# Optimization experiments

Measured on AMD Instinct MI355X. Metric: run time of the kernel, lower is better.

Reference implementation:

```python
import jax, jax.numpy as jnp
import numpy as np

EPS = 1e-5
HEADS = 8
SR = 4


def bn(x, gamma, beta, mean, var):
    # BatchNorm in inference form; channel axis = 1
    shape = (1, -1) + (1,) * (x.ndim - 2)
    inv = gamma.reshape(shape) / jnp.sqrt(var.reshape(shape) + EPS)
    return (x - mean.reshape(shape)) * inv + beta.reshape(shape)


def setup_inputs() -> dict:
    key = jax.random.key(0)
    ks = jax.random.split(key, 8)
    B, C, H, W = 2, 256, 128, 128
    N = H * W
    conv1d_std = np.sqrt(2.0 / C)            # fan_out = 1*C
    conv2d_std = np.sqrt(2.0 / (SR * SR * C))  # fan_out = sr*sr*C
    return {
        "x": jax.random.normal(ks[0], (B, C, N), dtype=jnp.float32),
        "w_q": jax.random.normal(ks[1], (C, C), dtype=jnp.float32) * conv1d_std,
        "w_k": jax.random.normal(ks[2], (C, C), dtype=jnp.float32) * conv1d_std,
        "w_sr": jax.random.normal(ks[3], (C, C, SR, SR), dtype=jnp.float32) * conv2d_std,
        "sr_gamma": jnp.ones((C,), jnp.float32),
        "sr_beta": jnp.zeros((C,), jnp.float32),
        "sr_mean": jnp.zeros((C,), jnp.float32),
        "sr_var": jnp.ones((C,), jnp.float32),
        "w_proj": jax.random.normal(ks[4], (C, C), dtype=jnp.float32) * conv1d_std,
        "proj_gamma": jnp.ones((C,), jnp.float32),
        "proj_beta": jnp.zeros((C,), jnp.float32),
        "proj_mean": jnp.zeros((C,), jnp.float32),
        "proj_var": jnp.ones((C,), jnp.float32),
        "H": 128,
        "W": 128,
    }


def reference(x, w_q, w_k, w_sr, sr_gamma, sr_beta, sr_mean, sr_var,
              w_proj, proj_gamma, proj_beta, proj_mean, proj_var, H, W):
    B, C, N = x.shape
    hd = C // HEADS
    scale = hd ** -0.5
    # q: Conv1d(k=1) == channel matmul -> (B, heads, N, hd)
    q = jnp.einsum('oc,bcn->bon', w_q, x).reshape(B, HEADS, hd, N).transpose(0, 1, 3, 2)
    # spatial reduction: Conv2d(k=SR, s=SR) as patch-reshape + einsum, then BN
    xp = x.reshape(B, C, H // SR, SR, W // SR, SR)
    xr = jnp.einsum('bchpwq,ocpq->bohw', xp, w_sr).reshape(B, C, (H // SR) * (W // SR))
    xr = bn(xr, sr_gamma, sr_beta, sr_mean, sr_var)
    # k: (B, heads, hd, N_kv)
    k = jnp.einsum('oc,bcm->bom', w_k, xr).reshape(B, HEADS, hd, -1)
    # scores (B, heads, N, N_kv) -> max over kv
    scores = jnp.einsum('bhnd,bhdm->bhnm', q, k) * scale
    attn = scores.max(axis=-1)                # (B, heads, N)
    # v = mean-pooled x, identical per head -> matmul collapses to sum over heads
    v = x.mean(axis=-1)                       # (B, C)
    out = jnp.einsum('bhn,bc->bcn', attn, v)  # (B, C, N)
    out = jnp.einsum('oc,bcn->bon', w_proj, out)
    return bn(out, proj_gamma, proj_beta, proj_mean, proj_var)
```

## Files before the change

### kernel.cpp

```cpp
#include <hip/hip_runtime.h>
#include <hip/hip_bf16.h>
#include <math.h>

#define EPSF 1e-5f
#define SCALE 0.17677669529663687f

typedef __bf16 bf16x8 __attribute__((ext_vector_type(8)));
typedef __bf16 bf16x4 __attribute__((ext_vector_type(4)));
typedef float f32x4 __attribute__((ext_vector_type(4)));


__global__ __launch_bounds__(256) void k_ab(const float* __restrict__ v,
                                            const float* __restrict__ wproj,
                                            const float* __restrict__ pg,
                                            const float* __restrict__ pb,
                                            const float* __restrict__ pm,
                                            const float* __restrict__ pvar,
                                            float* __restrict__ A,
                                            float* __restrict__ B0) {
    __shared__ float vl[256];
    int t = threadIdx.x, b = blockIdx.x;
    vl[t] = v[b * 256 + t] * (1.0f / 16384.0f);
    __syncthreads();
    const float* wr = wproj + t * 256;
    float s = 0.f;
#pragma unroll 8
    for (int c = 0; c < 256; c += 4) {
        float4 w = *(const float4*)&wr[c];
        s += w.x * vl[c] + w.y * vl[c + 1] + w.z * vl[c + 2] + w.w * vl[c + 3];
    }
    float inv = pg[t] / sqrtf(pvar[t] + EPSF);
    A[b * 256 + t] = s * inv;
    if (b == 0) B0[t] = pb[t] - pm[t] * inv;
}

__global__ __launch_bounds__(256) void k_wprep(const float* __restrict__ wq,
                                               const float* __restrict__ wk,
                                               const float* __restrict__ wsr,
                                               __bf16* __restrict__ wqf,
                                               __bf16* __restrict__ wkb,
                                               __bf16* __restrict__ wsrf,
                                               float* __restrict__ v) {
    int bi = blockIdx.x, t = threadIdx.x;
    if (bi < 32) {
        if (bi == 0) { v[t] = 0.f; v[256 + t] = 0.f; }
        int tt = bi * 256 + t;
        int o = tt >> 5, chunk = tt & 31;
        float4 v0 = *(const float4*)&wq[o * 256 + (chunk << 3)];
        float4 v1 = *(const float4*)&wq[o * 256 + (chunk << 3) + 4];
        bf16x8 p;
        p[0] = (__bf16)v0.x; p[1] = (__bf16)v0.y; p[2] = (__bf16)v0.z; p[3] = (__bf16)v0.w;
        p[4] = (__bf16)v1.x; p[5] = (__bf16)v1.y; p[6] = (__bf16)v1.z; p[7] = (__bf16)v1.w;
        int cc = chunk >> 2, quad = chunk & 3;
        *(bf16x8*)&wqf[(((((o >> 4) << 3) + cc) << 6) + (quad << 4) + (o & 15)) << 3] = p;
    } else if (bi < 64) {
        int e = (bi - 32) * 256 + t;
        float4 v0 = *(const float4*)&wk[e << 3];
        float4 v1 = *(const float4*)&wk[(e << 3) + 4];
        bf16x8 p;
        p[0] = (__bf16)(v0.x * SCALE); p[1] = (__bf16)(v0.y * SCALE);
        p[2] = (__bf16)(v0.z * SCALE); p[3] = (__bf16)(v0.w * SCALE);
        p[4] = (__bf16)(v1.x * SCALE); p[5] = (__bf16)(v1.y * SCALE);
        p[6] = (__bf16)(v1.z * SCALE); p[7] = (__bf16)(v1.w * SCALE);
        *(bf16x8*)&wkb[e << 3] = p;
    } else {
        int tt = (bi - 64) * 256 + t;
        int o = tt >> 9, chunk = tt & 511;
        float4 v0 = *(const float4*)&wsr[o * 4096 + (chunk << 3)];
        float4 v1 = *(const float4*)&wsr[o * 4096 + (chunk << 3) + 4];
        bf16x8 p;
        p[0] = (__bf16)v0.x; p[1] = (__bf16)v0.y; p[2] = (__bf16)v0.z; p[3] = (__bf16)v0.w;
        p[4] = (__bf16)v1.x; p[5] = (__bf16)v1.y; p[6] = (__bf16)v1.z; p[7] = (__bf16)v1.w;
        int cc = chunk >> 2, quad = chunk & 3;
        *(bf16x8*)&wsrf[(((((o >> 4) << 7) + cc) << 6) + (quad << 4) + (o & 15)) << 3] = p;
    }
}

__global__ __launch_bounds__(256) void k_im2col(const float* __restrict__ x,
                                                __bf16* __restrict__ Pbf,
                                                float* __restrict__ v) {
    __shared__ float csum[32];
    int t = threadIdx.x, bid = blockIdx.x;
    int b = bid >> 8, hm = (bid >> 3) & 31, ccg = bid & 7;
    int wm = t >> 3, c8 = t & 7;
    if (t < 32) csum[t] = 0.f;
    __syncthreads();
    const int mtile = (hm << 1) + (wm >> 4);
    const int ln = wm & 15;
#pragma unroll
    for (int cci = 0; cci < 4; ++cci) {
        int c = (ccg << 5) + (cci << 3) + c8;
        const float* src = x + ((size_t)(b * 256 + c) << 14) + (hm << 9) + (wm << 2);
        bf16x8 o0, o1;
        float s = 0.f;
#pragma unroll
        for (int p = 0; p < 2; ++p) {
            float4 vv = *(const float4*)&src[p << 7];
            s += vv.x + vv.y + vv.z + vv.w;
            o0[p * 4 + 0] = (__bf16)vv.x; o0[p * 4 + 1] = (__bf16)vv.y;
            o0[p * 4 + 2] = (__bf16)vv.z; o0[p * 4 + 3] = (__bf16)vv.w;
        }
#pragma unroll
        for (int p = 0; p < 2; ++p) {
            float4 vv = *(const float4*)&src[(p + 2) << 7];
            s += vv.x + vv.y + vv.z + vv.w;
            o1[p * 4 + 0] = (__bf16)vv.x; o1[p * 4 + 1] = (__bf16)vv.y;
            o1[p * 4 + 2] = (__bf16)vv.z; o1[p * 4 + 3] = (__bf16)vv.w;
        }
        size_t d0 = (((((size_t)(b * 64 + mtile) << 7) + (c >> 1)) << 6) +
                     (((c & 1) << 1) << 4) + ln) << 3;
        *(bf16x8*)&Pbf[d0] = o0;
        *(bf16x8*)&Pbf[d0 + 128] = o1;
        atomicAdd(&csum[(cci << 3) + c8], s);
    }
    __syncthreads();
    if (t < 32) atomicAdd(&v[b * 256 + (ccg << 5) + t], csum[t]);
}

__global__ __launch_bounds__(256) void k_conv1(const __bf16* __restrict__ Pbf,
                                               const __bf16* __restrict__ wsrf,
                                               float* __restrict__ xrp) {
    const int t = threadIdx.x, bid = blockIdx.x;
    const int b = bid & 1, mt = (bid >> 1) & 63, ks = bid >> 7;
    const int w = t >> 6, lane = t & 63, ln = lane & 15, quad = lane >> 4;
    f32x4 acc[4];
#pragma unroll
    for (int ot = 0; ot < 4; ++ot) acc[ot] = (f32x4){0.f, 0.f, 0.f, 0.f};
    const __bf16* pa = Pbf + ((((size_t)(b * 64 + mt) << 7) + (ks << 5)) << 9) + (lane << 3);
    const __bf16* pbm = wsrf + ((((size_t)(w << 2) << 7) + (ks << 5)) << 9) + (lane << 3);
#pragma unroll 4
    for (int cci = 0; cci < 32; ++cci) {
        const int cb = cci << 9;
        bf16x8 af = *(const bf16x8*)&pa[cb];
        bf16x8 bfr[4];
#pragma unroll
        for (int ot = 0; ot < 4; ++ot) bfr[ot] = *(const bf16x8*)&pbm[(ot << 16) + cb];
#pragma unroll
        for (int ot = 0; ot < 4; ++ot)
            acc[ot] = __builtin_amdgcn_mfma_f32_16x16x32_bf16(af, bfr[ot], acc[ot], 0, 0, 0);
    }
    float* dst = xrp + ((size_t)((ks << 1) + b) << 18);
#pragma unroll
    for (int ot = 0; ot < 4; ++ot)
#pragma unroll
        for (int r = 0; r < 4; ++r) {
            int m = (mt << 4) + (quad << 2) + r;
            int o = (w << 6) + (ot << 4) + ln;
            dst[m * 256 + o] = acc[ot][r];
        }
}

__global__ __launch_bounds__(256) void k_comb2(const float* __restrict__ xrp,
                                               const float* __restrict__ sg,
                                               const float* __restrict__ sb,
                                               const float* __restrict__ smn,
                                               const float* __restrict__ svar,
                                               __bf16* __restrict__ xrb) {
    int t = threadIdx.x, bid = blockIdx.x;
    int b = bid >> 8, m = ((bid & 255) << 2) + (t >> 6);
    int o4 = (t & 63) << 2;
    size_t base = (((size_t)b << 10) + m) << 8;
    float4 s0 = *(const float4*)&xrp[base + o4];
    float4 s1 = *(const float4*)&xrp[524288 + base + o4];
    float4 s2 = *(const float4*)&xrp[1048576 + base + o4];
    float4 s3 = *(const float4*)&xrp[1572864 + base + o4];
    float4 g = *(const float4*)&sg[o4];
    float4 vr = *(const float4*)&svar[o4];
    float4 mn = *(const float4*)&smn[o4];
    float4 bt = *(const float4*)&sb[o4];
    bf16x4 r;
    r[0] = (__bf16)((s0.x + s1.x + s2.x + s3.x - mn.x) * (g.x / sqrtf(vr.x + EPSF)) + bt.x);
    r[1] = (__bf16)((s0.y + s1.y + s2.y + s3.y - mn.y) * (g.y / sqrtf(vr.y + EPSF)) + bt.y);
    r[2] = (__bf16)((s0.z + s1.z + s2.z + s3.z - mn.z) * (g.z / sqrtf(vr.z + EPSF)) + bt.z);
    r[3] = (__bf16)((s0.w + s1.w + s2.w + s3.w - mn.w) * (g.w / sqrtf(vr.w + EPSF)) + bt.w);
    *(bf16x4*)&xrb[base + o4] = r;
}

__global__ __launch_bounds__(256) void k_kmat2(const __bf16* __restrict__ xrb,
                                               const __bf16* __restrict__ wkb,
                                               __bf16* __restrict__ kkbh) {
    const int t = threadIdx.x, bid = blockIdx.x;
    const int b = bid >> 6, mt = bid & 63;
    const int w = t >> 6, lane = t & 63, ln = lane & 15, quad = lane >> 4;
    f32x4 acc[4];
#pragma unroll
    for (int ot = 0; ot < 4; ++ot) acc[ot] = (f32x4){0.f, 0.f, 0.f, 0.f};
    const __bf16* pa = xrb + ((((size_t)b << 10) + (mt << 4) + ln) << 8) + (quad << 3);
    const __bf16* pbm = wkb + (((w << 6) + ln) << 8) + (quad << 3);
#pragma unroll
    for (int cc = 0; cc < 8; ++cc) {
        const int cb = cc << 5;
        bf16x8 af = *(const bf16x8*)&pa[cb];
        bf16x8 bfr[4];
#pragma unroll
        for (int ot = 0; ot < 4; ++ot) bfr[ot] = *(const bf16x8*)&pbm[(ot << 12) + cb];
#pragma unroll
        for (int ot = 0; ot < 4; ++ot)
            acc[ot] = __builtin_amdgcn_mfma_f32_16x16x32_bf16(af, bfr[ot], acc[ot], 0, 0, 0);
    }
#pragma unroll
    for (int ot = 0; ot < 4; ++ot)
#pragma unroll
        for (int r = 0; r < 4; ++r) {
            int m = (mt << 4) + (quad << 2) + r;
            int h = (w << 1) + (ot >> 1);
            int d = ((ot & 1) << 4) + ln;
            kkbh[(((size_t)(b * 8 + h)) << 15) + (m << 5) + d] = (__bf16)acc[ot][r];
        }
}

__global__ __launch_bounds__(256) void k_xt(const float* __restrict__ x,
                                            __bf16* __restrict__ xTf) {
    __shared__ float ts[32 * 68];
    int t = threadIdx.x, bid = blockIdx.x;
    int b = bid >> 8, n0 = (bid & 255) << 6;
    const int nl = t >> 2;
    const int ch = (t & 3) << 3;
    const int n = n0 + nl;
    const int ntile = n >> 4, ln = n & 15, quad = ch >> 3;
    const int cl = t >> 3;
    const int n8 = (t & 7) << 3;
    for (int s8 = 0; s8 < 8; ++s8) {
        int c0 = s8 << 5;
        __syncthreads();
        {
            const float* src = &x[((size_t)(b * 256 + c0 + cl) << 14) + n0 + n8];
            *(float4*)&ts[cl * 68 + n8] = *(const float4*)&src[0];
            *(float4*)&ts[cl * 68 + n8 + 4] = *(const float4*)&src[4];
        }
        __syncthreads();
        bf16x8 p;
#pragma unroll
        for (int j = 0; j < 8; ++j) p[j] = (__bf16)ts[(ch + j) * 68 + nl];
        *(bf16x8*)&xTf[(((((size_t)(b * 1024 + ntile) << 3) + s8) << 6) +
                        (quad << 4) + ln) << 3] = p;
    }
}

__global__ __launch_bounds__(256) void k_scores2(const __bf16* __restrict__ xTf,
                                                 const __bf16* __restrict__ wqf,
                                                 const __bf16* __restrict__ kkbh,
                                                 const float* __restrict__ A,
                                                 const float* __restrict__ B0,
                                                 float* __restrict__ out) {
    __shared__ __align__(16) __bf16 qs[64 * 264];
    __shared__ float smax[2048];
    __shared__ float ss[64];
    __shared__ float sA[256], sB[256];
    const int t = threadIdx.x;
    const int w = t >> 6;
    const int lane = t & 63;
    const int ln = lane & 15;
    const int quad = lane >> 4;
    const int b = blockIdx.x >> 8;
    const int n0 = (blockIdx.x & 255) << 6;

    f32x4 acc[4][4];
#pragma unroll
    for (int nt = 0; nt < 4; ++nt)
#pragma unroll
        for (int ot = 0; ot < 4; ++ot) acc[nt][ot] = (f32x4){0.f, 0.f, 0.f, 0.f};
    const __bf16* pa = xTf + (((size_t)(b * 1024 + (n0 >> 4))) << 12) + (lane << 3);
    const __bf16* pbm = wqf + ((size_t)w << 14) + (lane << 3);
#pragma unroll 2
    for (int cc = 0; cc < 8; ++cc) {
        const int cb = cc << 9;
        bf16x8 af[4], bfr[4];
#pragma unroll
        for (int nt = 0; nt < 4; ++nt) af[nt] = *(const bf16x8*)&pa[(nt << 12) + cb];
#pragma unroll
        for (int ot = 0; ot < 4; ++ot) bfr[ot] = *(const bf16x8*)&pbm[(ot << 12) + cb];
#pragma unroll
        for (int nt = 0; nt < 4; ++nt)
#pragma unroll
            for (int ot = 0; ot < 4; ++ot)
                acc[nt][ot] = __builtin_amdgcn_mfma_f32_16x16x32_bf16(af[nt], bfr[ot],
                                                                      acc[nt][ot], 0, 0, 0);
    }
#pragma unroll
    for (int nt = 0; nt < 4; ++nt)
#pragma unroll
        for (int ot = 0; ot < 4; ++ot)
#pragma unroll
            for (int r = 0; r < 4; ++r)
                qs[((nt << 4) + (quad << 2) + r) * 264 + (w << 6) + (ot << 4) + ln] =
                    (__bf16)acc[nt][ot][r];
    __syncthreads();

    const f32x4 zf = {0.f, 0.f, 0.f, 0.f};
    for (int h = 0; h < 8; ++h) {
        bf16x8 qb[4];
#pragma unroll
        for (int nt = 0; nt < 4; ++nt)
            qb[nt] = *(const bf16x8*)&qs[((nt << 4) + ln) * 264 + (h << 5) + (quad << 3)];
        const __bf16* kb_base = kkbh + ((size_t)(b * 8 + h) << 15) + (ln << 5) + (quad << 3);
        bf16x8 kb[16];
#pragma unroll
        for (int i = 0; i < 16; ++i)
            kb[i] = *(const bf16x8*)&kb_base[((w << 8) + (i << 4)) << 5];
        float rmx[4] = {-INFINITY, -INFINITY, -INFINITY, -INFINITY};
#pragma unroll
        for (int i = 0; i < 16; ++i)
#pragma unroll
            for (int nt = 0; nt < 4; ++nt) {
                f32x4 d = __builtin_amdgcn_mfma_f32_16x16x32_bf16(kb[i], qb[nt], zf, 0, 0, 0);
                rmx[nt] = fmaxf(rmx[nt], fmaxf(fmaxf(d[0], d[1]), fmaxf(d[2], d[3])));
            }
#pragma unroll
        for (int nt = 0; nt < 4; ++nt) {
            rmx[nt] = fmaxf(rmx[nt], __shfl_xor(rmx[nt], 16, 64));
            rmx[nt] = fmaxf(rmx[nt], __shfl_xor(rmx[nt], 32, 64));
        }
        if (lane < 16) {
#pragma unroll
            for (int nt = 0; nt < 4; ++nt)
                smax[(w << 9) + (h << 6) + (nt << 4) + lane] = rmx[nt];
        }
    }
    __syncthreads();
    if (t < 64) {
        float ssum = 0.f;
#pragma unroll
        for (int h = 0; h < 8; ++h) {
            float vv = fmaxf(fmaxf(smax[(h << 6) + t], smax[512 + (h << 6) + t]),
                             fmaxf(smax[1024 + (h << 6) + t], smax[1536 + (h << 6) + t]));
            ssum += vv;
        }
        ss[t] = ssum;
    }
    sA[t] = A[b * 256 + t];
    sB[t] = B0[t];
    __syncthreads();

#pragma unroll
    for (int i = 0; i < 16; ++i) {
        int e = t + (i << 8);
        int c = e >> 4, n4 = (e & 15) << 2;
        float4 s4 = *(const float4*)&ss[n4];
        float a = sA[c], bb = sB[c];
        float4 o4 = make_float4(fmaf(a, s4.x, bb), fmaf(a, s4.y, bb),
                                fmaf(a, s4.z, bb), fmaf(a, s4.w, bb));
        *(float4*)&out[((size_t)(b * 256 + c) << 14) + n0 + n4] = o4;
    }
}

extern "C" void kernel_launch(void* const* d_in, const int* in_sizes, int n_in,
                              void* d_out, int out_size, void* d_ws, size_t ws_size,
                              hipStream_t stream) {
    const float* x    = (const float*)d_in[0];
    const float* wq   = (const float*)d_in[1];
    const float* wk   = (const float*)d_in[2];
    const float* wsr  = (const float*)d_in[3];
    const float* sg   = (const float*)d_in[4];
    const float* sb   = (const float*)d_in[5];
    const float* smn  = (const float*)d_in[6];
    const float* svr  = (const float*)d_in[7];
    const float* wproj= (const float*)d_in[8];
    const float* pg   = (const float*)d_in[9];
    const float* pb   = (const float*)d_in[10];
    const float* pm   = (const float*)d_in[11];
    const float* pvr  = (const float*)d_in[12];
    float* out = (float*)d_out;

    char* W = (char*)d_ws;
    float*  w_v   = (float*) (W + 0);
    float*  w_A   = (float*) (W + 4096);
    float*  w_B0  = (float*) (W + 8192);
    __bf16* w_wqf = (__bf16*)(W + 16384);
    __bf16* w_wkb = (__bf16*)(W + 147456);
    __bf16* w_wsrf= (__bf16*)(W + 278528);
    __bf16* w_xrb = (__bf16*)(W + 2375680);
    __bf16* w_kkbh= (__bf16*)(W + 2899968);
    float*  w_xrp = (float*) (W + 3948544);
    __bf16* w_Pbf = (__bf16*)(W + 12337152);
    __bf16* w_xTf = (__bf16*)(W + 12337152);

    k_wprep<<<576, 256, 0, stream>>>(wq, wk, wsr, w_wqf, w_wkb, w_wsrf, w_v);
    k_im2col<<<512, 256, 0, stream>>>(x, w_Pbf, w_v);
    k_ab<<<2, 256, 0, stream>>>(w_v, wproj, pg, pb, pm, pvr, w_A, w_B0);
    k_conv1<<<512, 256, 0, stream>>>(w_Pbf, w_wsrf, w_xrp);
    k_comb2<<<512, 256, 0, stream>>>(w_xrp, sg, sb, smn, svr, w_xrb);
    k_kmat2<<<128, 256, 0, stream>>>(w_xrb, w_wkb, w_kkbh);
    k_xt<<<512, 256, 0, stream>>>(x, w_xTf);
    k_scores2<<<512, 256, 0, stream>>>(w_xTf, w_wqf, w_kkbh, w_A, w_B0, out);
}
```

Before: 194.8 us.

## Merge staging kernels, fuse conv BN, split scores by head pairs

Merges im2col and the x transpose into one launch, and folds the projection-vector kernel into the k-matrix kernel. The conv now runs its full K reduction per block with BN applied in the epilogue, which removes the fp32 partial buffer and the combine kernel. Scores are split four ways across head pairs to raise block count, with per-head maxima summed through global atomics into a zeroed buffer. A separate epilogue kernel then writes the output. The cost is that each head-pair block recomputes the q projection for its slice, and atomics plus an extra launch are added.

```diff
diff --git a/kernel.cpp b/kernel.cpp
--- a/kernel.cpp
+++ b/kernel.cpp
@@ -9,30 +9,6 @@
 typedef __bf16 bf16x4 __attribute__((ext_vector_type(4)));
 typedef float f32x4 __attribute__((ext_vector_type(4)));
 
-
-__global__ __launch_bounds__(256) void k_ab(const float* __restrict__ v,
-                                            const float* __restrict__ wproj,
-                                            const float* __restrict__ pg,
-                                            const float* __restrict__ pb,
-                                            const float* __restrict__ pm,
-                                            const float* __restrict__ pvar,
-                                            float* __restrict__ A,
-                                            float* __restrict__ B0) {
-    __shared__ float vl[256];
-    int t = threadIdx.x, b = blockIdx.x;
-    vl[t] = v[b * 256 + t] * (1.0f / 16384.0f);
-    __syncthreads();
-    const float* wr = wproj + t * 256;
-    float s = 0.f;
-#pragma unroll 8
-    for (int c = 0; c < 256; c += 4) {
-        float4 w = *(const float4*)&wr[c];
-        s += w.x * vl[c] + w.y * vl[c + 1] + w.z * vl[c + 2] + w.w * vl[c + 3];
-    }
-    float inv = pg[t] / sqrtf(pvar[t] + EPSF);
-    A[b * 256 + t] = s * inv;
-    if (b == 0) B0[t] = pb[t] - pm[t] * inv;
-}
 
 __global__ __launch_bounds__(256) void k_wprep(const float* __restrict__ wq,
                                                const float* __restrict__ wk,
@@ -40,8 +16,14 @@
                                                __bf16* __restrict__ wqf,
                                                __bf16* __restrict__ wkb,
                                                __bf16* __restrict__ wsrf,
-                                               float* __restrict__ v) {
+                                               float* __restrict__ v,
+                                               float* __restrict__ ssg) {
     int bi = blockIdx.x, t = threadIdx.x;
+    if (bi >= 576) {
+        int e = (bi - 576) * 256 + t;
+        *(float4*)&ssg[e << 2] = make_float4(0.f, 0.f, 0.f, 0.f);
+        return;
+    }
     if (bi < 32) {
         if (bi == 0) { v[t] = 0.f; v[256 + t] = 0.f; }
         int tt = bi * 256 + t;
@@ -76,110 +58,134 @@
     }
 }
 
-__global__ __launch_bounds__(256) void k_im2col(const float* __restrict__ x,
-                                                __bf16* __restrict__ Pbf,
-                                                float* __restrict__ v) {
-    __shared__ float csum[32];
-    int t = threadIdx.x, bid = blockIdx.x;
-    int b = bid >> 8, hm = (bid >> 3) & 31, ccg = bid & 7;
-    int wm = t >> 3, c8 = t & 7;
-    if (t < 32) csum[t] = 0.f;
-    __syncthreads();
-    const int mtile = (hm << 1) + (wm >> 4);
-    const int ln = wm & 15;
-#pragma unroll
-    for (int cci = 0; cci < 4; ++cci) {
-        int c = (ccg << 5) + (cci << 3) + c8;
-        const float* src = x + ((size_t)(b * 256 + c) << 14) + (hm << 9) + (wm << 2);
-        bf16x8 o0, o1;
-        float s = 0.f;
-#pragma unroll
-        for (int p = 0; p < 2; ++p) {
-            float4 vv = *(const float4*)&src[p << 7];
-            s += vv.x + vv.y + vv.z + vv.w;
-            o0[p * 4 + 0] = (__bf16)vv.x; o0[p * 4 + 1] = (__bf16)vv.y;
-            o0[p * 4 + 2] = (__bf16)vv.z; o0[p * 4 + 3] = (__bf16)vv.w;
-        }
-#pragma unroll
-        for (int p = 0; p < 2; ++p) {
-            float4 vv = *(const float4*)&src[(p + 2) << 7];
-            s += vv.x + vv.y + vv.z + vv.w;
-            o1[p * 4 + 0] = (__bf16)vv.x; o1[p * 4 + 1] = (__bf16)vv.y;
-            o1[p * 4 + 2] = (__bf16)vv.z; o1[p * 4 + 3] = (__bf16)vv.w;
-        }
-        size_t d0 = (((((size_t)(b * 64 + mtile) << 7) + (c >> 1)) << 6) +
-                     (((c & 1) << 1) << 4) + ln) << 3;
-        *(bf16x8*)&Pbf[d0] = o0;
-        *(bf16x8*)&Pbf[d0 + 128] = o1;
-        atomicAdd(&csum[(cci << 3) + c8], s);
-    }
-    __syncthreads();
-    if (t < 32) atomicAdd(&v[b * 256 + (ccg << 5) + t], csum[t]);
-}
-
-__global__ __launch_bounds__(256) void k_conv1(const __bf16* __restrict__ Pbf,
-                                               const __bf16* __restrict__ wsrf,
-                                               float* __restrict__ xrp) {
+__global__ __launch_bounds__(256) void k_stage(const float* __restrict__ x,
+                                               __bf16* __restrict__ Pbf,
+                                               __bf16* __restrict__ xTf,
+                                               float* __restrict__ v) {
+    int t = threadIdx.x, bid0 = blockIdx.x;
+    if (bid0 < 512) {
+        __shared__ float csum[32];
+        int bid = bid0;
+        int b = bid >> 8, hm = (bid >> 3) & 31, ccg = bid & 7;
+        int wm = t >> 3, c8 = t & 7;
+        if (t < 32) csum[t] = 0.f;
+        __syncthreads();
+        const int mtile = (hm << 1) + (wm >> 4);
+        const int ln = wm & 15;
+#pragma unroll
+        for (int cci = 0; cci < 4; ++cci) {
+            int c = (ccg << 5) + (cci << 3) + c8;
+            const float* src = x + ((size_t)(b * 256 + c) << 14) + (hm << 9) + (wm << 2);
+            bf16x8 o0, o1;
+            float s = 0.f;
+#pragma unroll
+            for (int p = 0; p < 2; ++p) {
+                float4 vv = *(const float4*)&src[p << 7];
+                s += vv.x + vv.y + vv.z + vv.w;
+                o0[p * 4 + 0] = (__bf16)vv.x; o0[p * 4 + 1] = (__bf16)vv.y;
+                o0[p * 4 + 2] = (__bf16)vv.z; o0[p * 4 + 3] = (__bf16)vv.w;
+            }
+#pragma unroll
+            for (int p = 0; p < 2; ++p) {
+                float4 vv = *(const float4*)&src[(p + 2) << 7];
+                s += vv.x + vv.y + vv.z + vv.w;
+                o1[p * 4 + 0] = (__bf16)vv.x; o1[p * 4 + 1] = (__bf16)vv.y;
+                o1[p * 4 + 2] = (__bf16)vv.z; o1[p * 4 + 3] = (__bf16)vv.w;
+            }
+            size_t d0 = (((((size_t)(b * 64 + mtile) << 7) + (c >> 1)) << 6) +
+                         (((c & 1) << 1) << 4) + ln) << 3;
+            *(bf16x8*)&Pbf[d0] = o0;
+            *(bf16x8*)&Pbf[d0 + 128] = o1;
+            atomicAdd(&csum[(cci << 3) + c8], s);
+        }
+        __syncthreads();
+        if (t < 32) atomicAdd(&v[b * 256 + (ccg << 5) + t], csum[t]);
+    } else {
+        __shared__ float ts[32 * 68];
+        int bid = bid0 - 512;
+        int b = bid >> 8, n0 = (bid & 255) << 6;
+        const int nl = t >> 2;
+        const int ch = (t & 3) << 3;
+        const int n = n0 + nl;
+        const int ntile = n >> 4, ln = n & 15, quad = ch >> 3;
+        const int cl = t >> 3;
+        const int n8 = (t & 7) << 3;
+        for (int s8 = 0; s8 < 8; ++s8) {
+            int c0 = s8 << 5;
+            __syncthreads();
+            {
+                const float* src = &x[((size_t)(b * 256 + c0 + cl) << 14) + n0 + n8];
+                *(float4*)&ts[cl * 68 + n8] = *(const float4*)&src[0];
+                *(float4*)&ts[cl * 68 + n8 + 4] = *(const float4*)&src[4];
+            }
+            __syncthreads();
+            bf16x8 p;
+#pragma unroll
+            for (int j = 0; j < 8; ++j) p[j] = (__bf16)ts[(ch + j) * 68 + nl];
+            *(bf16x8*)&xTf[(((((size_t)(b * 1024 + ntile) << 3) + s8) << 6) +
+                            (quad << 4) + ln) << 3] = p;
+        }
+    }
+}
+
+__global__ __launch_bounds__(256) void k_conv1f(const __bf16* __restrict__ Pbf,
+                                                const __bf16* __restrict__ wsrf,
+                                                const float* __restrict__ sg,
+                                                const float* __restrict__ sb,
+                                                const float* __restrict__ smn,
+                                                const float* __restrict__ svar,
+                                                __bf16* __restrict__ xrb) {
     const int t = threadIdx.x, bid = blockIdx.x;
-    const int b = bid & 1, mt = (bid >> 1) & 63, ks = bid >> 7;
+    const int b = bid & 1, mt = (bid >> 1) & 63, og = bid >> 7;
     const int w = t >> 6, lane = t & 63, ln = lane & 15, quad = lane >> 4;
-    f32x4 acc[4];
-#pragma unroll
-    for (int ot = 0; ot < 4; ++ot) acc[ot] = (f32x4){0.f, 0.f, 0.f, 0.f};
-    const __bf16* pa = Pbf + ((((size_t)(b * 64 + mt) << 7) + (ks << 5)) << 9) + (lane << 3);
-    const __bf16* pbm = wsrf + ((((size_t)(w << 2) << 7) + (ks << 5)) << 9) + (lane << 3);
-#pragma unroll 4
-    for (int cci = 0; cci < 32; ++cci) {
-        const int cb = cci << 9;
-        bf16x8 af = *(const bf16x8*)&pa[cb];
-        bf16x8 bfr[4];
-#pragma unroll
-        for (int ot = 0; ot < 4; ++ot) bfr[ot] = *(const bf16x8*)&pbm[(ot << 16) + cb];
-#pragma unroll
-        for (int ot = 0; ot < 4; ++ot)
-            acc[ot] = __builtin_amdgcn_mfma_f32_16x16x32_bf16(af, bfr[ot], acc[ot], 0, 0, 0);
-    }
-    float* dst = xrp + ((size_t)((ks << 1) + b) << 18);
-#pragma unroll
-    for (int ot = 0; ot < 4; ++ot)
-#pragma unroll
-        for (int r = 0; r < 4; ++r) {
-            int m = (mt << 4) + (quad << 2) + r;
-            int o = (w << 6) + (ot << 4) + ln;
-            dst[m * 256 + o] = acc[ot][r];
-        }
-}
-
-__global__ __launch_bounds__(256) void k_comb2(const float* __restrict__ xrp,
-                                               const float* __restrict__ sg,
-                                               const float* __restrict__ sb,
-                                               const float* __restrict__ smn,
-                                               const float* __restrict__ svar,
-                                               __bf16* __restrict__ xrb) {
-    int t = threadIdx.x, bid = blockIdx.x;
-    int b = bid >> 8, m = ((bid & 255) << 2) + (t >> 6);
-    int o4 = (t & 63) << 2;
-    size_t base = (((size_t)b << 10) + m) << 8;
-    float4 s0 = *(const float4*)&xrp[base + o4];
-    float4 s1 = *(const float4*)&xrp[524288 + base + o4];
-    float4 s2 = *(const float4*)&xrp[1048576 + base + o4];
-    float4 s3 = *(const float4*)&xrp[1572864 + base + o4];
-    float4 g = *(const float4*)&sg[o4];
-    float4 vr = *(const float4*)&svar[o4];
-    float4 mn = *(const float4*)&smn[o4];
-    float4 bt = *(const float4*)&sb[o4];
-    bf16x4 r;
-    r[0] = (__bf16)((s0.x + s1.x + s2.x + s3.x - mn.x) * (g.x / sqrtf(vr.x + EPSF)) + bt.x);
-    r[1] = (__bf16)((s0.y + s1.y + s2.y + s3.y - mn.y) * (g.y / sqrtf(vr.y + EPSF)) + bt.y);
-    r[2] = (__bf16)((s0.z + s1.z + s2.z + s3.z - mn.z) * (g.z / sqrtf(vr.z + EPSF)) + bt.z);
-    r[3] = (__bf16)((s0.w + s1.w + s2.w + s3.w - mn.w) * (g.w / sqrtf(vr.w + EPSF)) + bt.w);
-    *(bf16x4*)&xrb[base + o4] = r;
+    f32x4 acc = (f32x4){0.f, 0.f, 0.f, 0.f};
+    const __bf16* pa = Pbf + ((size_t)(b * 64 + mt) << 16) + (lane << 3);
+    const __bf16* pbm = wsrf + ((size_t)(og * 4 + w) << 16) + (lane << 3);
+#pragma unroll 8
+    for (int cc = 0; cc < 128; ++cc) {
+        bf16x8 af = *(const bf16x8*)&pa[cc << 9];
+        bf16x8 bf = *(const bf16x8*)&pbm[cc << 9];
+        acc = __builtin_amdgcn_mfma_f32_16x16x32_bf16(af, bf, acc, 0, 0, 0);
+    }
+    const int o = (og << 6) + (w << 4) + ln;
+    float inv = sg[o] / sqrtf(svar[o] + EPSF);
+    float mn = smn[o], bt = sb[o];
+#pragma unroll
+    for (int r = 0; r < 4; ++r) {
+        int m = (mt << 4) + (quad << 2) + r;
+        xrb[(((size_t)b << 10) + m) * 256 + o] = (__bf16)((acc[r] - mn) * inv + bt);
+    }
 }
 
 __global__ __launch_bounds__(256) void k_kmat2(const __bf16* __restrict__ xrb,
                                                const __bf16* __restrict__ wkb,
-                                               __bf16* __restrict__ kkbh) {
+                                               __bf16* __restrict__ kkbh,
+                                               const float* __restrict__ v,
+                                               const float* __restrict__ wproj,
+                                               const float* __restrict__ pg,
+                                               const float* __restrict__ pb,
+                                               const float* __restrict__ pm,
+                                               const float* __restrict__ pvar,
+                                               float* __restrict__ A,
+                                               float* __restrict__ B0) {
     const int t = threadIdx.x, bid = blockIdx.x;
+    if (bid >= 128) {
+        __shared__ float vl[256];
+        int b = bid - 128;
+        vl[t] = v[b * 256 + t] * (1.0f / 16384.0f);
+        __syncthreads();
+        const float* wr = wproj + t * 256;
+        float s = 0.f;
+#pragma unroll 8
+        for (int c = 0; c < 256; c += 4) {
+            float4 w4 = *(const float4*)&wr[c];
+            s += w4.x * vl[c] + w4.y * vl[c + 1] + w4.z * vl[c + 2] + w4.w * vl[c + 3];
+        }
+        float inv = pg[t] / sqrtf(pvar[t] + EPSF);
+        A[b * 256 + t] = s * inv;
+        if (b == 0) B0[t] = pb[t] - pm[t] * inv;
+        return;
+    }
     const int b = bid >> 6, mt = bid & 63;
     const int w = t >> 6, lane = t & 63, ln = lane & 15, quad = lane >> 4;
     f32x4 acc[4];
@@ -209,90 +215,53 @@
         }
 }
 
-__global__ __launch_bounds__(256) void k_xt(const float* __restrict__ x,
-                                            __bf16* __restrict__ xTf) {
-    __shared__ float ts[32 * 68];
-    int t = threadIdx.x, bid = blockIdx.x;
-    int b = bid >> 8, n0 = (bid & 255) << 6;
-    const int nl = t >> 2;
-    const int ch = (t & 3) << 3;
-    const int n = n0 + nl;
-    const int ntile = n >> 4, ln = n & 15, quad = ch >> 3;
-    const int cl = t >> 3;
-    const int n8 = (t & 7) << 3;
-    for (int s8 = 0; s8 < 8; ++s8) {
-        int c0 = s8 << 5;
-        __syncthreads();
-        {
-            const float* src = &x[((size_t)(b * 256 + c0 + cl) << 14) + n0 + n8];
-            *(float4*)&ts[cl * 68 + n8] = *(const float4*)&src[0];
-            *(float4*)&ts[cl * 68 + n8 + 4] = *(const float4*)&src[4];
-        }
-        __syncthreads();
-        bf16x8 p;
-#pragma unroll
-        for (int j = 0; j < 8; ++j) p[j] = (__bf16)ts[(ch + j) * 68 + nl];
-        *(bf16x8*)&xTf[(((((size_t)(b * 1024 + ntile) << 3) + s8) << 6) +
-                        (quad << 4) + ln) << 3] = p;
-    }
-}
-
 __global__ __launch_bounds__(256) void k_scores2(const __bf16* __restrict__ xTf,
                                                  const __bf16* __restrict__ wqf,
                                                  const __bf16* __restrict__ kkbh,
-                                                 const float* __restrict__ A,
-                                                 const float* __restrict__ B0,
-                                                 float* __restrict__ out) {
-    __shared__ __align__(16) __bf16 qs[64 * 264];
-    __shared__ float smax[2048];
-    __shared__ float ss[64];
-    __shared__ float sA[256], sB[256];
+                                                 float* __restrict__ ssg) {
+    __shared__ __align__(16) __bf16 qs[64 * 72];
+    __shared__ float smax[512];
     const int t = threadIdx.x;
     const int w = t >> 6;
     const int lane = t & 63;
     const int ln = lane & 15;
     const int quad = lane >> 4;
-    const int b = blockIdx.x >> 8;
-    const int n0 = (blockIdx.x & 255) << 6;
-
-    f32x4 acc[4][4];
-#pragma unroll
-    for (int nt = 0; nt < 4; ++nt)
-#pragma unroll
-        for (int ot = 0; ot < 4; ++ot) acc[nt][ot] = (f32x4){0.f, 0.f, 0.f, 0.f};
-    const __bf16* pa = xTf + (((size_t)(b * 1024 + (n0 >> 4))) << 12) + (lane << 3);
-    const __bf16* pbm = wqf + ((size_t)w << 14) + (lane << 3);
+    const int bx = blockIdx.x;
+    const int hp = bx & 3;
+    const int n0 = ((bx >> 2) & 255) << 6;
+    const int b = bx >> 10;
+
+    f32x4 acc[4];
+#pragma unroll
+    for (int ot = 0; ot < 4; ++ot) acc[ot] = (f32x4){0.f, 0.f, 0.f, 0.f};
+    const __bf16* pa = xTf + ((size_t)(b * 1024 + (n0 >> 4) + w) << 12) + (lane << 3);
+    const __bf16* pbm = wqf + ((size_t)(hp << 2) << 12) + (lane << 3);
 #pragma unroll 2
     for (int cc = 0; cc < 8; ++cc) {
         const int cb = cc << 9;
-        bf16x8 af[4], bfr[4];
-#pragma unroll
-        for (int nt = 0; nt < 4; ++nt) af[nt] = *(const bf16x8*)&pa[(nt << 12) + cb];
+        bf16x8 af = *(const bf16x8*)&pa[cb];
+        bf16x8 bfr[4];
 #pragma unroll
         for (int ot = 0; ot < 4; ++ot) bfr[ot] = *(const bf16x8*)&pbm[(ot << 12) + cb];
 #pragma unroll
+        for (int ot = 0; ot < 4; ++ot)
+            acc[ot] = __builtin_amdgcn_mfma_f32_16x16x32_bf16(af, bfr[ot], acc[ot], 0, 0, 0);
+    }
+#pragma unroll
+    for (int ot = 0; ot < 4; ++ot)
+#pragma unroll
+        for (int r = 0; r < 4; ++r)
+            qs[((w << 4) + (quad << 2) + r) * 72 + (ot << 4) + ln] = (__bf16)acc[ot][r];
+    __syncthreads();
+
+    const f32x4 zf = {0.f, 0.f, 0.f, 0.f};
+#pragma unroll
+    for (int hl = 0; hl < 2; ++hl) {
+        const int h = (hp << 1) + hl;
+        bf16x8 qb[4];
+#pragma unroll
         for (int nt = 0; nt < 4; ++nt)
-#pragma unroll
-            for (int ot = 0; ot < 4; ++ot)
-                acc[nt][ot] = __builtin_amdgcn_mfma_f32_16x16x32_bf16(af[nt], bfr[ot],
-                                                                      acc[nt][ot], 0, 0, 0);
-    }
-#pragma unroll
-    for (int nt = 0; nt < 4; ++nt)
-#pragma unroll
-        for (int ot = 0; ot < 4; ++ot)
-#pragma unroll
-            for (int r = 0; r < 4; ++r)
-                qs[((nt << 4) + (quad << 2) + r) * 264 + (w << 6) + (ot << 4) + ln] =
-                    (__bf16)acc[nt][ot][r];
-    __syncthreads();
-
-    const f32x4 zf = {0.f, 0.f, 0.f, 0.f};
-    for (int h = 0; h < 8; ++h) {
-        bf16x8 qb[4];
-#pragma unroll
-        for (int nt = 0; nt < 4; ++nt)
-            qb[nt] = *(const bf16x8*)&qs[((nt << 4) + ln) * 264 + (h << 5) + (quad << 3)];
+            qb[nt] = *(const bf16x8*)&qs[((nt << 4) + ln) * 72 + (hl << 5) + (quad << 3)];
         const __bf16* kb_base = kkbh + ((size_t)(b * 8 + h) << 15) + (ln << 5) + (quad << 3);
         bf16x8 kb[16];
 #pragma unroll
@@ -304,7 +273,8 @@
 #pragma unroll
             for (int nt = 0; nt < 4; ++nt) {
                 f32x4 d = __builtin_amdgcn_mfma_f32_16x16x32_bf16(kb[i], qb[nt], zf, 0, 0, 0);
-                rmx[nt] = fmaxf(rmx[nt], fmaxf(fmaxf(d[0], d[1]), fmaxf(d[2], d[3])));
+                float t1 = fmaxf(fmaxf(d[0], d[1]), d[2]);
+                rmx[nt] = fmaxf(fmaxf(t1, d[3]), rmx[nt]);
             }
 #pragma unroll
         for (int nt = 0; nt < 4; ++nt) {
@@ -314,24 +284,29 @@
         if (lane < 16) {
 #pragma unroll
             for (int nt = 0; nt < 4; ++nt)
-                smax[(w << 9) + (h << 6) + (nt << 4) + lane] = rmx[nt];
+                smax[(w << 7) + (hl << 6) + (nt << 4) + lane] = rmx[nt];
         }
     }
     __syncthreads();
     if (t < 64) {
-        float ssum = 0.f;
-#pragma unroll
-        for (int h = 0; h < 8; ++h) {
-            float vv = fmaxf(fmaxf(smax[(h << 6) + t], smax[512 + (h << 6) + t]),
-                             fmaxf(smax[1024 + (h << 6) + t], smax[1536 + (h << 6) + t]));
-            ssum += vv;
-        }
-        ss[t] = ssum;
-    }
+        float s0 = fmaxf(fmaxf(smax[t], smax[128 + t]), fmaxf(smax[256 + t], smax[384 + t]));
+        float s1 = fmaxf(fmaxf(smax[64 + t], smax[192 + t]),
+                         fmaxf(smax[320 + t], smax[448 + t]));
+        atomicAdd(&ssg[(b << 14) + n0 + t], s0 + s1);
+    }
+}
+
+__global__ __launch_bounds__(256) void k_epi(const float* __restrict__ ssg,
+                                             const float* __restrict__ A,
+                                             const float* __restrict__ B0,
+                                             float* __restrict__ out) {
+    __shared__ float ss[64], sA[256], sB[256];
+    const int t = threadIdx.x, bid = blockIdx.x;
+    const int b = bid >> 8, n0 = (bid & 255) << 6;
+    if (t < 64) ss[t] = ssg[(b << 14) + n0 + t];
     sA[t] = A[b * 256 + t];
     sB[t] = B0[t];
     __syncthreads();
-
 #pragma unroll
     for (int i = 0; i < 16; ++i) {
         int e = t + (i << 8);
@@ -366,21 +341,20 @@
     float*  w_v   = (float*) (W + 0);
     float*  w_A   = (float*) (W + 4096);
     float*  w_B0  = (float*) (W + 8192);
-    __bf16* w_wqf = (__bf16*)(W + 16384);
-    __bf16* w_wkb = (__bf16*)(W + 147456);
-    __bf16* w_wsrf= (__bf16*)(W + 278528);
-    __bf16* w_xrb = (__bf16*)(W + 2375680);
-    __bf16* w_kkbh= (__bf16*)(W + 2899968);
-    float*  w_xrp = (float*) (W + 3948544);
-    __bf16* w_Pbf = (__bf16*)(W + 12337152);
-    __bf16* w_xTf = (__bf16*)(W + 12337152);
-
-    k_wprep<<<576, 256, 0, stream>>>(wq, wk, wsr, w_wqf, w_wkb, w_wsrf, w_v);
-    k_im2col<<<512, 256, 0, stream>>>(x, w_Pbf, w_v);
-    k_ab<<<2, 256, 0, stream>>>(w_v, wproj, pg, pb, pm, pvr, w_A, w_B0);
-    k_conv1<<<512, 256, 0, stream>>>(w_Pbf, w_wsrf, w_xrp);
-    k_comb2<<<512, 256, 0, stream>>>(w_xrp, sg, sb, smn, svr, w_xrb);
-    k_kmat2<<<128, 256, 0, stream>>>(w_xrb, w_wkb, w_kkbh);
-    k_xt<<<512, 256, 0, stream>>>(x, w_xTf);
-    k_scores2<<<512, 256, 0, stream>>>(w_xTf, w_wqf, w_kkbh, w_A, w_B0, out);
-}
+    float*  w_ssg = (float*) (W + 12288);
+    __bf16* w_wqf = (__bf16*)(W + 147456);
+    __bf16* w_wkb = (__bf16*)(W + 278528);
+    __bf16* w_wsrf= (__bf16*)(W + 409600);
+    __bf16* w_xrb = (__bf16*)(W + 2506752);
+    __bf16* w_kkbh= (__bf16*)(W + 3031040);
+    __bf16* w_Pbf = (__bf16*)(W + 4079616);
+    __bf16* w_xTf = (__bf16*)(W + 20856832);
+
+    k_wprep<<<608, 256, 0, stream>>>(wq, wk, wsr, w_wqf, w_wkb, w_wsrf, w_v, w_ssg);
+    k_stage<<<1024, 256, 0, stream>>>(x, w_Pbf, w_xTf, w_v);
+    k_conv1f<<<512, 256, 0, stream>>>(w_Pbf, w_wsrf, sg, sb, smn, svr, w_xrb);
+    k_kmat2<<<130, 256, 0, stream>>>(w_xrb, w_wkb, w_kkbh, w_v, wproj, pg, pb, pm, pvr,
+                                     w_A, w_B0);
+    k_scores2<<<2048, 256, 0, stream>>>(w_xTf, w_wqf, w_kkbh, w_ssg);
+    k_epi<<<512, 256, 0, stream>>>(w_ssg, w_A, w_B0, out);
+}
```

Result: no change. 191.4 us (-1.7%).
